# Kernel tuning notes

Measured on AMD Instinct MI355X. Metric: run time of the kernel, lower is better.

Reference implementation:

```python
import jax, jax.numpy as jnp
import numpy as np

N_NODES = 100000
N_EDGES = 1600000
IN_FEATS = 128
H1 = 256
H2 = 256
N_CLASSES = 64


def setup_inputs() -> dict:
    key = jax.random.key(0)
    ks = jax.random.split(key, 12)
    x = jax.random.normal(ks[0], (N_NODES, IN_FEATS), dtype=jnp.float32)
    src = jax.random.randint(ks[1], (N_EDGES,), 0, N_NODES, dtype=jnp.int64 if jax.config.jax_enable_x64 else jnp.int32)
    dst = jax.random.randint(ks[2], (N_EDGES,), 0, N_NODES, dtype=jnp.int64 if jax.config.jax_enable_x64 else jnp.int32)
    def lin(kw, kb, fan_in, fan_out):
        bound = 1.0 / np.sqrt(fan_in)
        W = jax.random.uniform(kw, (fan_out, fan_in), minval=-bound, maxval=bound, dtype=jnp.float32)
        b = jax.random.uniform(kb, (fan_out,), minval=-bound, maxval=bound, dtype=jnp.float32)
        return W, b
    W1, b1 = lin(ks[3], ks[4], 2 * IN_FEATS, H1)
    W2, b2 = lin(ks[5], ks[6], 2 * H1, H2)
    W3, b3 = lin(ks[7], ks[8], 2 * H2, N_CLASSES)
    return {"x": x, "src": src, "dst": dst,
            "W1": W1, "b1": b1, "W2": W2, "b2": b2, "W3": W3, "b3": b3}


def _sage_conv(h, src, dst, W, b):
    # message = copy from src node, reduce = mean at dst node (DGL copy_u + mean)
    m = jnp.take(h, src, axis=0)                                  # [E, d]
    s = jax.ops.segment_sum(m, dst, num_segments=N_NODES)         # [N, d]
    deg = jax.ops.segment_sum(jnp.ones((m.shape[0],), h.dtype), dst,
                              num_segments=N_NODES)               # [N]
    h_N = s / jnp.maximum(deg, 1.0)[:, None]                      # isolated nodes -> 0 (DGL behavior)
    h_total = jnp.concatenate([h, h_N], axis=1)                   # [N, 2d]
    return h_total @ W.T + b                                      # dropout inactive at eval (p=0.05)


def reference(x, src, dst, W1, b1, W2, b2, W3, b3):
    h = jax.nn.relu(_sage_conv(x, src, dst, W1, b1))
    h = jax.nn.relu(_sage_conv(h, src, dst, W2, b2))
    return _sage_conv(h, src, dst, W3, b3)
```

## Files before the change

kernel.cpp:

```cpp
#include <hip/hip_runtime.h>
#include <hip/hip_bf16.h>
#include <cstdint>
#include <cstddef>

#define N_NODES 100000
#define N_EDGES 1600000
#define NBUCK   256
#define NPB     391
#define NB_E    ((N_EDGES + 4095) / 4096)

#define MID_P   NB_E
#define MID_X   (MID_P + 12500)
#define MID_W1  (MID_X + 64)
#define MID_W2  (MID_W1 + 128)
#define MID_END (MID_W2 + 32)

typedef __attribute__((ext_vector_type(8))) short short8;
typedef __attribute__((ext_vector_type(4))) float floatx4;

__device__ inline float bf_lo(unsigned int u) { return __uint_as_float(u << 16); }
__device__ inline float bf_hi(unsigned int u) { return __uint_as_float(u & 0xffff0000u); }
__device__ inline unsigned short f2bf(float f) {
  unsigned int u = __float_as_uint(f);
  u += 0x7fffu + ((u >> 16) & 1u);
  return (unsigned short)(u >> 16);
}

__device__ inline void cvt4_body(const float* __restrict__ in,
                                 unsigned short* __restrict__ out, int t) {
  float4 v = ((const float4*)in)[t];
  ushort4 o;
  o.x = f2bf(v.x); o.y = f2bf(v.y); o.z = f2bf(v.z); o.w = f2bf(v.w);
  ((ushort4*)out)[t] = o;
}

__global__ __launch_bounds__(256)
void pass1a_kernel(const int* __restrict__ dst, int* __restrict__ blockHist) {
  __shared__ int hist[NBUCK];
  const int b = blockIdx.x, tid = threadIdx.x;
  hist[tid] = 0;
  __syncthreads();
#pragma unroll
  for (int i = 0; i < 16; ++i) {
    int e = b * 4096 + i * 256 + tid;
    if (e < N_EDGES) atomicAdd(&hist[dst[e] / NPB], 1);
  }
  __syncthreads();
  blockHist[b * NBUCK + tid] = hist[tid];
}

__device__ inline int wave_incl_scan(int v, int lane) {
#pragma unroll
  for (int off = 1; off < 64; off <<= 1) {
    int t = __shfl_up(v, off, 64);
    if (lane >= off) v += t;
  }
  return v;
}

__global__ __launch_bounds__(256)
void scanB1_kernel(const int* __restrict__ blockHist,
                   int* __restrict__ blockOfs, int* __restrict__ bucketCount) {
  int bucket = (int)((blockIdx.x * 256 + threadIdx.x) >> 6);
  if (bucket >= NBUCK) return;
  int lane = threadIdx.x & 63;
  int carry = 0;
  for (int c0 = 0; c0 < NB_E; c0 += 64) {
    int blk = c0 + lane;
    int v = (blk < NB_E) ? blockHist[blk * NBUCK + bucket] : 0;
    int incl = wave_incl_scan(v, lane);
    if (blk < NB_E) blockOfs[blk * NBUCK + bucket] = carry + incl - v;
    carry += __shfl(incl, 63, 64);
  }
  if (lane == 63) bucketCount[bucket] = carry;
}

__global__ void scanB2_kernel(const int* __restrict__ bucketCount,
                              int* __restrict__ bucketBase) {
  __shared__ int wsum[4];
  int t = threadIdx.x, lane = t & 63, wid = t >> 6;
  int v = bucketCount[t];
  int incl = wave_incl_scan(v, lane);
  if (lane == 63) wsum[wid] = incl;
  __syncthreads();
  int off = 0;
  for (int w = 0; w < wid; ++w) off += wsum[w];
  bucketBase[t] = off + incl - v;
  if (t == NBUCK - 1) bucketBase[NBUCK] = off + incl;
}

__global__ __launch_bounds__(256)
void mid_kernel(const int* __restrict__ src, const int* __restrict__ dst,
                const int* __restrict__ blockOfs, const int* __restrict__ bucketBase,
                unsigned int* __restrict__ staging,
                const float* __restrict__ x,  unsigned short* __restrict__ H0,
                const float* __restrict__ W1, unsigned short* __restrict__ Wb1,
                const float* __restrict__ W2, unsigned short* __restrict__ Wb2,
                const float* __restrict__ W3, unsigned short* __restrict__ Wb3) {
  __shared__ int hist[NBUCK];
  const int b = blockIdx.x, tid = threadIdx.x;
  if (b < MID_P) {
    hist[tid] = bucketBase[tid] + blockOfs[b * NBUCK + tid];
    __syncthreads();
#pragma unroll
    for (int i = 0; i < 16; ++i) {
      int e = b * 4096 + i * 256 + tid;
      if (e < N_EDGES) {
        int d = dst[e];
        int bb = d / NPB;
        int pos = atomicAdd(&hist[bb], 1);
        staging[pos] = (unsigned)src[e] | ((unsigned)(d - bb * NPB) << 17);
      }
    }
  } else if (b < MID_X) {
    cvt4_body(x, H0, (b - MID_P) * 256 + tid);
  } else if (b < MID_W1) {
    cvt4_body(W1, Wb1, (b - MID_X) * 256 + tid);
  } else if (b < MID_W2) {
    cvt4_body(W2, Wb2, (b - MID_W1) * 256 + tid);
  } else {
    int t = (b - MID_W2) * 256 + tid;
    int idx4 = t * 4;
    int r = idx4 >> 8, c = idx4 & 255;
    float4 v = *(const float4*)(W3 + (size_t)(r & 63) * 512 + (r >> 6) * 256 + c);
    ushort4 o;
    o.x = f2bf(v.x); o.y = f2bf(v.y); o.z = f2bf(v.z); o.w = f2bf(v.w);
    *(ushort4*)(Wb3 + (size_t)r * 256 + c) = o;
  }
}

__global__ __launch_bounds__(512)
void pass2_kernel(const unsigned int* __restrict__ staging, const int* __restrict__ bucketBase,
                  int* __restrict__ start, float* __restrict__ invdeg,
                  int* __restrict__ esrc) {
  __shared__ int cnt[512];
  __shared__ int cur[512];
  __shared__ int wsum[8];
  const int b = blockIdx.x, tid = threadIdx.x;
  const int lane = tid & 63, wid = tid >> 6;
  const int n0 = b * NPB, n1 = min(n0 + NPB, N_NODES);
  const int nLocal = n1 - n0;
  const int p0 = bucketBase[b], p1 = bucketBase[b + 1];

  cnt[tid] = 0;
  __syncthreads();
  for (int e = p0 + tid; e < p1; e += 512)
    atomicAdd(&cnt[staging[e] >> 17], 1);
  __syncthreads();

  int c = cnt[tid];
  int incl = wave_incl_scan(c, lane);
  if (lane == 63) wsum[wid] = incl;
  __syncthreads();
  if (wid == 0) {
    int v = (lane < 8) ? wsum[lane] : 0;
    int i2 = wave_incl_scan(v, lane);
    if (lane < 8) wsum[lane] = i2 - v;
  }
  __syncthreads();
  int excl = wsum[wid] + incl - c;
  cur[tid] = excl;
  if (tid < nLocal) {
    start[n0 + tid] = p0 + excl;
    invdeg[n0 + tid] = 1.0f / fmaxf((float)c, 1.0f);
  }
  if (b == NBUCK - 1 && tid == 0) start[N_NODES] = N_EDGES;
  __syncthreads();

  for (int e = p0 + tid; e < p1; e += 512) {
    unsigned int pr = staging[e];
    int pos = p0 + atomicAdd(&cur[pr >> 17], 1);
    esrc[pos] = (int)(pr & 0x1FFFFu);
  }
}

template<int D>
__global__ __launch_bounds__(256)
void gather_mean(const unsigned short* __restrict__ h,
                 const int* __restrict__ start,
                 const int* __restrict__ esrc,
                 const float* __restrict__ invdeg,
                 unsigned short* __restrict__ hn) {
  int wave = (int)((blockIdx.x * 256 + threadIdx.x) >> 6);
  if (wave >= N_NODES) return;
  int lane = threadIdx.x & 63;
  int s0 = start[wave], s1 = start[wave + 1];
  constexpr int FPL = D / 64;
  float acc[FPL] = {};
  const unsigned short* base = h + lane * FPL;

  int e = s0;
  if constexpr (FPL == 4) {
    for (; e + 4 <= s1; e += 4) {
      int sn0 = esrc[e], sn1 = esrc[e + 1], sn2 = esrc[e + 2], sn3 = esrc[e + 3];
      uint2 p0 = *(const uint2*)(base + (size_t)sn0 * D);
      uint2 p1 = *(const uint2*)(base + (size_t)sn1 * D);
      uint2 p2 = *(const uint2*)(base + (size_t)sn2 * D);
      uint2 p3 = *(const uint2*)(base + (size_t)sn3 * D);
      acc[0] += bf_lo(p0.x) + bf_lo(p1.x) + bf_lo(p2.x) + bf_lo(p3.x);
      acc[1] += bf_hi(p0.x) + bf_hi(p1.x) + bf_hi(p2.x) + bf_hi(p3.x);
      acc[2] += bf_lo(p0.y) + bf_lo(p1.y) + bf_lo(p2.y) + bf_lo(p3.y);
      acc[3] += bf_hi(p0.y) + bf_hi(p1.y) + bf_hi(p2.y) + bf_hi(p3.y);
    }
    for (; e < s1; ++e) {
      int sn = esrc[e];
      uint2 p = *(const uint2*)(base + (size_t)sn * D);
      acc[0] += bf_lo(p.x); acc[1] += bf_hi(p.x);
      acc[2] += bf_lo(p.y); acc[3] += bf_hi(p.y);
    }
  } else {
    for (; e + 4 <= s1; e += 4) {
      int sn0 = esrc[e], sn1 = esrc[e + 1], sn2 = esrc[e + 2], sn3 = esrc[e + 3];
      unsigned int p0 = *(const unsigned int*)(base + (size_t)sn0 * D);
      unsigned int p1 = *(const unsigned int*)(base + (size_t)sn1 * D);
      unsigned int p2 = *(const unsigned int*)(base + (size_t)sn2 * D);
      unsigned int p3 = *(const unsigned int*)(base + (size_t)sn3 * D);
      acc[0] += bf_lo(p0) + bf_lo(p1) + bf_lo(p2) + bf_lo(p3);
      acc[1] += bf_hi(p0) + bf_hi(p1) + bf_hi(p2) + bf_hi(p3);
    }
    for (; e < s1; ++e) {
      int sn = esrc[e];
      unsigned int p = *(const unsigned int*)(base + (size_t)sn * D);
      acc[0] += bf_lo(p); acc[1] += bf_hi(p);
    }
  }

  float inv = invdeg[wave];
  unsigned short* out = hn + (size_t)wave * D + lane * FPL;
  if constexpr (FPL == 4) {
    ushort4 o;
    o.x = f2bf(acc[0] * inv); o.y = f2bf(acc[1] * inv);
    o.z = f2bf(acc[2] * inv); o.w = f2bf(acc[3] * inv);
    *(ushort4*)out = o;
  } else {
    ushort2 o;
    o.x = f2bf(acc[0] * inv); o.y = f2bf(acc[1] * inv);
    *(ushort2*)out = o;
  }
}

__global__ __launch_bounds__(256)
void gather_add64(const unsigned short* __restrict__ Y3,
                  const int* __restrict__ start, const int* __restrict__ esrc,
                  const float* __restrict__ invdeg, float* __restrict__ out) {
  int wave = (int)((blockIdx.x * 256 + threadIdx.x) >> 6);
  if (wave >= N_NODES) return;
  int lane = threadIdx.x & 63;
  int slot = lane >> 4, l16 = lane & 15;
  int s0 = start[wave], s1 = start[wave + 1];
  const unsigned short* ybase = Y3 + 4 * l16;
  float a0 = 0.f, a1 = 0.f, a2 = 0.f, a3 = 0.f;
  int e = s0 + slot;
  for (; e + 12 < s1; e += 16) {
    int sn0 = esrc[e], sn1 = esrc[e + 4], sn2 = esrc[e + 8], sn3 = esrc[e + 12];
    uint2 p0 = *(const uint2*)(ybase + (size_t)sn0 * 64);
    uint2 p1 = *(const uint2*)(ybase + (size_t)sn1 * 64);
    uint2 p2 = *(const uint2*)(ybase + (size_t)sn2 * 64);
    uint2 p3 = *(const uint2*)(ybase + (size_t)sn3 * 64);
    a0 += bf_lo(p0.x) + bf_lo(p1.x) + bf_lo(p2.x) + bf_lo(p3.x);
    a1 += bf_hi(p0.x) + bf_hi(p1.x) + bf_hi(p2.x) + bf_hi(p3.x);
    a2 += bf_lo(p0.y) + bf_lo(p1.y) + bf_lo(p2.y) + bf_lo(p3.y);
    a3 += bf_hi(p0.y) + bf_hi(p1.y) + bf_hi(p2.y) + bf_hi(p3.y);
  }
  for (; e < s1; e += 4) {
    uint2 p = *(const uint2*)(ybase + (size_t)esrc[e] * 64);
    a0 += bf_lo(p.x); a1 += bf_hi(p.x);
    a2 += bf_lo(p.y); a3 += bf_hi(p.y);
  }
  a0 += __shfl_xor(a0, 16, 64); a1 += __shfl_xor(a1, 16, 64);
  a2 += __shfl_xor(a2, 16, 64); a3 += __shfl_xor(a3, 16, 64);
  a0 += __shfl_xor(a0, 32, 64); a1 += __shfl_xor(a1, 32, 64);
  a2 += __shfl_xor(a2, 32, 64); a3 += __shfl_xor(a3, 32, 64);
  if (slot == 0) {
    float inv = invdeg[wave];
    float4* q = (float4*)(out + (size_t)wave * 64 + 4 * l16);
    float4 v = *q;
    v.x += inv * a0; v.y += inv * a1; v.z += inv * a2; v.w += inv * a3;
    *q = v;
  }
}

template<int D, int DOUT, int BN, bool RELU, bool OUTF32, int MODE>
__global__ __launch_bounds__(256)
void sage_gemm(const unsigned short* __restrict__ H,
               const unsigned short* __restrict__ HN,
               const unsigned short* __restrict__ Wb,
               const float* __restrict__ bias,
               void* __restrict__ outp,
               unsigned short* __restrict__ y3) {
  constexpr int K   = (MODE == 1) ? D : 2 * D;
  constexpr int BM  = 128, KC = 32;
  constexpr int NCHUNK = K / KC;
  constexpr int AF  = BM / 16;
  constexpr int BF  = BN / 16;
  constexpr int FR  = AF + BF;
  constexpr int NMF = 4;
  constexpr int NJF = BF / 2;

  __shared__ __align__(16) unsigned short lds0[FR * 512];
  __shared__ __align__(16) unsigned short lds1[FR * 512];

  const int tid  = threadIdx.x;
  const int wave = tid >> 6, lane = tid & 63;
  const int l16  = lane & 15, quad = lane >> 4;
  const int n0   = blockIdx.y * BM;
  const int bn0  = blockIdx.x * BN;
  const int wm   = wave >> 1, wn = wave & 1;

  floatx4 acc[NMF][NJF] = {};

  auto stage = [&](int c, unsigned short* buf) {
    const int kc = c * KC;
    const unsigned short* srcH = (kc < D) ? H : HN;
    const int kb = (kc < D) ? kc : kc - D;
    const int w0 = __builtin_amdgcn_readfirstlane(wave);
#pragma unroll
    for (int i = 0; i < FR / 4; ++i) {
      const int fu = w0 + 4 * i;
      const unsigned short* g;
      if (fu < AF) {
        int row = min(n0 + fu * 16 + l16, N_NODES - 1);
        g = srcH + (size_t)row * D + kb + quad * 8;
      } else {
        int col = bn0 + (fu - AF) * 16 + l16;
        g = Wb + (size_t)col * K + kc + quad * 8;
      }
      __builtin_amdgcn_global_load_lds(
          (const __attribute__((address_space(1))) unsigned int*)g,
          (__attribute__((address_space(3))) unsigned int*)(buf + fu * 512),
          16, 0, 0);
    }
  };

  auto compute = [&](const unsigned short* buf) {
    short8 b[NJF];
#pragma unroll
    for (int jt = 0; jt < NJF; ++jt)
      b[jt] = *(const short8*)(buf + (AF + wn * NJF + jt) * 512 + lane * 8);
#pragma unroll
    for (int mi = 0; mi < NMF; ++mi) {
      short8 a = *(const short8*)(buf + (wm * NMF + mi) * 512 + lane * 8);
#pragma unroll
      for (int jt = 0; jt < NJF; ++jt)
        acc[mi][jt] = __builtin_amdgcn_mfma_f32_16x16x32_bf16(a, b[jt], acc[mi][jt], 0, 0, 0);
    }
  };

  stage(0, lds0);
  __syncthreads();
#pragma unroll 1
  for (int c = 0; c < NCHUNK; c += 2) {
    stage(c + 1, lds1);
    compute(lds0);
    __syncthreads();
    if (c + 2 < NCHUNK) stage(c + 2, lds0);
    compute(lds1);
    __syncthreads();
  }

#pragma unroll
  for (int mi = 0; mi < NMF; ++mi) {
#pragma unroll
    for (int jt = 0; jt < NJF; ++jt) {
      int j = bn0 + wn * (NJF * 16) + jt * 16 + l16;
      float bj = (MODE == 1 && wn == 1) ? 0.0f : bias[j];
#pragma unroll
      for (int r = 0; r < 4; ++r) {
        int node = n0 + wm * 64 + mi * 16 + quad * 4 + r;
        if (node < N_NODES) {
          float v = acc[mi][jt][r];
          if constexpr (MODE == 1) {
            if (wn == 0) ((float*)outp)[(size_t)node * 64 + j] = v + bj;
            else y3[(size_t)node * 64 + (j - 64)] = f2bf(v);
          } else {
            v += bj;
            if (RELU) v = fmaxf(v, 0.0f);
            if (OUTF32) ((float*)outp)[(size_t)node * DOUT + j] = v;
            else ((unsigned short*)outp)[(size_t)node * DOUT + j] = f2bf(v);
          }
        }
      }
    }
  }
}

extern "C" void kernel_launch(void* const* d_in, const int* in_sizes, int n_in,
                              void* d_out, int out_size, void* d_ws, size_t ws_size,
                              hipStream_t stream) {
  const float* x   = (const float*)d_in[0];
  const int*   src = (const int*)d_in[1];
  const int*   dst = (const int*)d_in[2];
  const float* W1 = (const float*)d_in[3];
  const float* b1 = (const float*)d_in[4];
  const float* W2 = (const float*)d_in[5];
  const float* b2 = (const float*)d_in[6];
  const float* W3 = (const float*)d_in[7];
  const float* b3 = (const float*)d_in[8];

  char* ws = (char*)d_ws;
  unsigned short* H0 = (unsigned short*)ws; ws += (size_t)N_NODES * 128 * 2;
  unsigned short* H1 = (unsigned short*)ws; ws += (size_t)N_NODES * 256 * 2;
  unsigned short* H2 = (unsigned short*)ws; ws += (size_t)N_NODES * 256 * 2;
  unsigned short* HN = (unsigned short*)ws; ws += (size_t)N_NODES * 256 * 2;
  unsigned int* staging = (unsigned int*)ws; ws += (size_t)N_EDGES * 4;
  int* esrc   = (int*)ws;  ws += (size_t)N_EDGES * 4;
  int* startp = (int*)ws;  ws += (size_t)(N_NODES + 32) * 4;
  float* invdeg = (float*)ws; ws += (size_t)(N_NODES + 32) * 4;
  int* bucketBase  = (int*)ws; ws += (NBUCK + 32) * 4;
  int* bucketCount = (int*)ws; ws += NBUCK * 4;
  int* blockHist   = (int*)ws; ws += (size_t)NB_E * NBUCK * 4;
  int* blockOfs    = (int*)ws; ws += (size_t)NB_E * NBUCK * 4;
  unsigned short* Y3 = (unsigned short*)ws; ws += (size_t)N_NODES * 64 * 2;
  unsigned short* Wb1 = (unsigned short*)ws; ws += 256 * 256 * 2;
  unsigned short* Wb2 = (unsigned short*)ws; ws += 256 * 512 * 2;
  unsigned short* Wb3 = (unsigned short*)ws; ws += 128 * 256 * 2;

  pass1a_kernel<<<NB_E, 256, 0, stream>>>(dst, blockHist);
  scanB1_kernel<<<(NBUCK * 64 + 255) / 256, 256, 0, stream>>>(blockHist, blockOfs, bucketCount);
  scanB2_kernel<<<1, NBUCK, 0, stream>>>(bucketCount, bucketBase);
  mid_kernel<<<MID_END, 256, 0, stream>>>(src, dst, blockOfs, bucketBase, staging,
                                          x, H0, W1, Wb1, W2, Wb2, W3, Wb3);
  pass2_kernel<<<NBUCK, 512, 0, stream>>>(staging, bucketBase, startp, invdeg, esrc);

  const int GGRID = (N_NODES * 64 + 255) / 256;
  const int MG = (N_NODES + 127) / 128;

  gather_mean<128><<<GGRID, 256, 0, stream>>>(H0, startp, esrc, invdeg, HN);
  sage_gemm<128, 256, 128, true, false, 0><<<dim3(2, MG), 256, 0, stream>>>(H0, HN, Wb1, b1, H1, nullptr);

  gather_mean<256><<<GGRID, 256, 0, stream>>>(H1, startp, esrc, invdeg, HN);
  sage_gemm<256, 256, 128, true, false, 0><<<dim3(2, MG), 256, 0, stream>>>(H1, HN, Wb2, b2, H2, nullptr);

  sage_gemm<256, 128, 128, false, true, 1><<<dim3(1, MG), 256, 0, stream>>>(H2, nullptr, Wb3, b3, (float*)d_out, Y3);
  gather_add64<<<GGRID, 256, 0, stream>>>(Y3, startp, esrc, invdeg, (float*)d_out);
}
```

Before: 555.0 us.

## Quantize layer-1 activations to fp8 for the layer-2 neighbor gather

The layer-1 GEMM epilogue now also writes a custom positive-only 8-bit float copy of the post-ReLU activations into the H2 buffer region. A new gather kernel reads these 1-byte values, decodes them by bit shifting and scaling, and computes the neighbor mean. This halves the bytes moved by the random-access gather in layer 2, which is bandwidth bound. The cost is an extra byte store per element in the GEMM and a large precision loss (about 3 mantissa bits, with small values flushed to zero), which risks exceeding the accuracy tolerance.

```diff
diff --git a/kernel.cpp b/kernel.cpp
--- a/kernel.cpp
+++ b/kernel.cpp
@@ -24,6 +24,15 @@
   unsigned int u = __float_as_uint(f);
   u += 0x7fffu + ((u >> 16) & 1u);
   return (unsigned short)(u >> 16);
+}
+
+__device__ inline unsigned int f2fp8_pos(float v) {
+  unsigned int b = __float_as_uint(v);
+  b += 0x7ffffu + ((b >> 20) & 1u);
+  int q = (int)(b >> 20) - 960;
+  q = (q < 8) ? 0 : q;
+  q = (q > 0x7e) ? 0x7e : q;
+  return (unsigned int)q;
 }
 
 __device__ inline void cvt4_body(const float* __restrict__ in,
@@ -237,6 +246,59 @@
     o.x = f2bf(acc[0] * inv); o.y = f2bf(acc[1] * inv);
     *(ushort2*)out = o;
   }
+}
+
+__global__ __launch_bounds__(256)
+void gather_mean_fp8(const unsigned char* __restrict__ hq,
+                     const int* __restrict__ start,
+                     const int* __restrict__ esrc,
+                     const float* __restrict__ invdeg,
+                     unsigned short* __restrict__ hn) {
+  int wave = (int)((blockIdx.x * 256 + threadIdx.x) >> 6);
+  if (wave >= N_NODES) return;
+  int lane = threadIdx.x & 63;
+  int s0 = start[wave], s1 = start[wave + 1];
+  const float S = 0x1p120f;
+  float a0 = 0.f, a1 = 0.f, a2 = 0.f, a3 = 0.f;
+  const unsigned char* base = hq + lane * 4;
+
+  int e = s0;
+  for (; e + 4 <= s1; e += 4) {
+    int sn0 = esrc[e], sn1 = esrc[e + 1], sn2 = esrc[e + 2], sn3 = esrc[e + 3];
+    unsigned int p0 = *(const unsigned int*)(base + (size_t)sn0 * 256);
+    unsigned int p1 = *(const unsigned int*)(base + (size_t)sn1 * 256);
+    unsigned int p2 = *(const unsigned int*)(base + (size_t)sn2 * 256);
+    unsigned int p3 = *(const unsigned int*)(base + (size_t)sn3 * 256);
+    a0 += __uint_as_float((p0 << 20) & 0x07f00000u) * S
+        + __uint_as_float((p1 << 20) & 0x07f00000u) * S
+        + __uint_as_float((p2 << 20) & 0x07f00000u) * S
+        + __uint_as_float((p3 << 20) & 0x07f00000u) * S;
+    a1 += __uint_as_float((p0 << 12) & 0x07f00000u) * S
+        + __uint_as_float((p1 << 12) & 0x07f00000u) * S
+        + __uint_as_float((p2 << 12) & 0x07f00000u) * S
+        + __uint_as_float((p3 << 12) & 0x07f00000u) * S;
+    a2 += __uint_as_float((p0 << 4)  & 0x07f00000u) * S
+        + __uint_as_float((p1 << 4)  & 0x07f00000u) * S
+        + __uint_as_float((p2 << 4)  & 0x07f00000u) * S
+        + __uint_as_float((p3 << 4)  & 0x07f00000u) * S;
+    a3 += __uint_as_float((p0 >> 4)  & 0x07f00000u) * S
+        + __uint_as_float((p1 >> 4)  & 0x07f00000u) * S
+        + __uint_as_float((p2 >> 4)  & 0x07f00000u) * S
+        + __uint_as_float((p3 >> 4)  & 0x07f00000u) * S;
+  }
+  for (; e < s1; ++e) {
+    unsigned int p = *(const unsigned int*)(base + (size_t)esrc[e] * 256);
+    a0 += __uint_as_float((p << 20) & 0x07f00000u) * S;
+    a1 += __uint_as_float((p << 12) & 0x07f00000u) * S;
+    a2 += __uint_as_float((p << 4)  & 0x07f00000u) * S;
+    a3 += __uint_as_float((p >> 4)  & 0x07f00000u) * S;
+  }
+
+  float inv = invdeg[wave];
+  ushort4 o;
+  o.x = f2bf(a0 * inv); o.y = f2bf(a1 * inv);
+  o.z = f2bf(a2 * inv); o.w = f2bf(a3 * inv);
+  *(ushort4*)(hn + (size_t)wave * 256 + lane * 4) = o;
 }
 
 __global__ __launch_bounds__(256)
@@ -376,7 +438,11 @@
             v += bj;
             if (RELU) v = fmaxf(v, 0.0f);
             if (OUTF32) ((float*)outp)[(size_t)node * DOUT + j] = v;
-            else ((unsigned short*)outp)[(size_t)node * DOUT + j] = f2bf(v);
+            else {
+              ((unsigned short*)outp)[(size_t)node * DOUT + j] = f2bf(v);
+              if (y3 != nullptr)
+                ((unsigned char*)y3)[(size_t)node * DOUT + j] = (unsigned char)f2fp8_pos(v);
+            }
           }
         }
       }
@@ -400,6 +466,7 @@
   char* ws = (char*)d_ws;
   unsigned short* H0 = (unsigned short*)ws; ws += (size_t)N_NODES * 128 * 2;
   unsigned short* H1 = (unsigned short*)ws; ws += (size_t)N_NODES * 256 * 2;
+  unsigned char*  H1q = (unsigned char*)ws;
   unsigned short* H2 = (unsigned short*)ws; ws += (size_t)N_NODES * 256 * 2;
   unsigned short* HN = (unsigned short*)ws; ws += (size_t)N_NODES * 256 * 2;
   unsigned int* staging = (unsigned int*)ws; ws += (size_t)N_EDGES * 4;
@@ -426,9 +493,9 @@
   const int MG = (N_NODES + 127) / 128;
 
   gather_mean<128><<<GGRID, 256, 0, stream>>>(H0, startp, esrc, invdeg, HN);
-  sage_gemm<128, 256, 128, true, false, 0><<<dim3(2, MG), 256, 0, stream>>>(H0, HN, Wb1, b1, H1, nullptr);
-
-  gather_mean<256><<<GGRID, 256, 0, stream>>>(H1, startp, esrc, invdeg, HN);
+  sage_gemm<128, 256, 128, true, false, 0><<<dim3(2, MG), 256, 0, stream>>>(H0, HN, Wb1, b1, H1, (unsigned short*)H1q);
+
+  gather_mean_fp8<<<GGRID, 256, 0, stream>>>(H1q, startp, esrc, invdeg, HN);
   sage_gemm<256, 256, 128, true, false, 0><<<dim3(2, MG), 256, 0, stream>>>(H1, HN, Wb2, b2, H2, nullptr);
 
   sage_gemm<256, 128, 128, false, true, 1><<<dim3(1, MG), 256, 0, stream>>>(H2, nullptr, Wb3, b3, (float*)d_out, Y3);
```

New measurement: 528.0 us. 4.9% less time.
